# Optimization experiments

Measured on AMD Instinct MI355X. Metric: run time of the kernel, lower is better.

Reference implementation:

```python
import jax, jax.numpy as jnp
import numpy as np

# Dimensions (see shape_source)
S = 32          # frames
P = 196         # tokens per frame (14x14 patches)
H = 16          # heads
D = 64          # head dim
C = H * D       # 1024
N = S * P       # 6272
B = 1
K_NEAREST = 10
MK = K_NEAREST * P  # max gathered KV tokens per frame (padded)
LN_EPS = 1e-6


def _build_covis_gather(rng):
    """Build [S, MK] gather indices + padding bias from a ragged covisibility mask,
    mirroring SparseAttentionAggregator._build_gather_index."""
    gather_idx = np.zeros((S, MK), dtype=np.int32)
    attn_bias = np.zeros((S, MK), dtype=np.float32)
    arange_p = np.arange(P)
    for i in range(S):
        k_i = int(rng.integers(4, K_NEAREST + 1))  # variable-size covisible set
        others = rng.choice(np.delete(np.arange(S), i), size=k_i - 1, replace=False)
        covis = np.sort(np.concatenate([[i], others]))  # always includes self
        tok = (covis[:, None] * P + arange_p[None, :]).reshape(-1)  # [k_i*P]
        gather_idx[i, : tok.size] = tok
        if tok.size < MK:
            gather_idx[i, tok.size:] = tok[0]   # pad with a valid token
            attn_bias[i, tok.size:] = -1e9      # mask padded positions
    return gather_idx, attn_bias


def setup_inputs() -> dict:
    key = jax.random.key(0)
    kx, kqkv, kproj = jax.random.split(key, 3)
    rng = np.random.default_rng(0)
    gather_idx, attn_bias = _build_covis_gather(rng)
    w_scale = 0.02
    return {
        "x": jax.random.normal(kx, (B, N, C), dtype=jnp.float32),
        "W_qkv": w_scale * jax.random.normal(kqkv, (C, 3 * C), dtype=jnp.float32),
        "b_qkv": jnp.zeros((3 * C,), dtype=jnp.float32),
        "q_gamma": jnp.ones((D,), dtype=jnp.float32),
        "q_beta": jnp.zeros((D,), dtype=jnp.float32),
        "k_gamma": jnp.ones((D,), dtype=jnp.float32),
        "k_beta": jnp.zeros((D,), dtype=jnp.float32),
        "W_proj": w_scale * jax.random.normal(kproj, (C, C), dtype=jnp.float32),
        "b_proj": jnp.zeros((C,), dtype=jnp.float32),
        "gather_idx": jnp.asarray(gather_idx),
        "attn_bias": jnp.asarray(attn_bias),
    }


def _layernorm(t, gamma, beta):
    # LayerNorm over the last (head) dim, as q_norm / k_norm
    mu = jnp.mean(t, axis=-1, keepdims=True)
    var = jnp.mean(jnp.square(t - mu), axis=-1, keepdims=True)
    return (t - mu) * jax.lax.rsqrt(var + LN_EPS) * gamma + beta


def reference(x, W_qkv, b_qkv, q_gamma, q_beta, k_gamma, k_beta, W_proj, b_proj,
              gather_idx, attn_bias):
    Bx, Nx, Cx = x.shape
    mk = gather_idx.shape[1]
    # qkv projection -> q, k, v as [B, H, N, D]
    qkv = (x @ W_qkv + b_qkv).reshape(Bx, Nx, 3, H, D)
    q = jnp.transpose(qkv[:, :, 0], (0, 2, 1, 3))
    k = jnp.transpose(qkv[:, :, 1], (0, 2, 1, 3))
    v = jnp.transpose(qkv[:, :, 2], (0, 2, 1, 3))
    q = _layernorm(q, q_gamma, q_beta)
    k = _layernorm(k, k_gamma, k_beta)
    # single gather of all covisible K/V tokens: [B, H, S*MK, D] -> [B, S, H, MK, D]
    flat_idx = gather_idx.reshape(-1)
    kf = jnp.transpose(k[:, :, flat_idx, :].reshape(Bx, H, S, mk, D), (0, 2, 1, 3, 4))
    vf = jnp.transpose(v[:, :, flat_idx, :].reshape(Bx, H, S, mk, D), (0, 2, 1, 3, 4))
    # queries grouped per frame: [B, S, H, P, D]
    qb = jnp.transpose(q.reshape(Bx, H, S, P, D), (0, 2, 1, 3, 4))
    # batched SDPA over all frames at once
    scores = jnp.einsum('bshpd,bshmd->bshpm', qb, kf) * (D ** -0.5)
    scores = scores + attn_bias[None, :, None, None, :]
    attn = jax.nn.softmax(scores, axis=-1)
    out = jnp.einsum('bshpm,bshmd->bshpd', attn, vf)  # [B, S, H, P, D]
    # back to [B, N, C]
    out = jnp.transpose(out, (0, 2, 1, 3, 4)).reshape(Bx, H, Nx, D)
    out = jnp.transpose(out, (0, 2, 1, 3)).reshape(Bx, Nx, Cx)
    return out @ W_proj + b_proj
```

## Files before the change

### kernel.cpp

```cpp
#include <hip/hip_runtime.h>
#include <hip/hip_bf16.h>
#include <cstdint>
#include <cstddef>

#define S_FRAMES 32
#define P_TOK    196
#define H_HEADS  16
#define D_HEAD   64
#define C_DIM    1024
#define N_TOK    (S_FRAMES * P_TOK)
#define MK_TOK   1960
#define LN_EPS   1e-6f
#define SM_SCALE 0.125f

typedef __attribute__((ext_vector_type(8))) short short8;
typedef __attribute__((ext_vector_type(4))) short short4v;
typedef __attribute__((ext_vector_type(4))) float f32x4;

static __device__ __forceinline__ ushort f2bf(float x) {
  union { float f; unsigned u; } c; c.f = x;
  unsigned r = (c.u + 0x7FFFu + ((c.u >> 16) & 1u)) >> 16;
  return (ushort)r;
}
static __device__ __forceinline__ float bf2f(ushort h) {
  union { unsigned u; float f; } c; c.u = ((unsigned)h) << 16;
  return c.f;
}
static __device__ __forceinline__ unsigned pack_bf16x2(float a, float b) {
  union { float f; unsigned u; } x, y; x.f = a; y.f = b;
  unsigned lo = (x.u + 0x7FFFu + ((x.u >> 16) & 1u)) >> 16;
  unsigned hi = (y.u + 0x7FFFu + ((y.u >> 16) & 1u)) >> 16;
  return lo | (hi << 16);
}

#define GLOAD16(g, l) __builtin_amdgcn_global_load_lds( \
    (const __attribute__((address_space(1))) void*)(g), \
    (__attribute__((address_space(3))) void*)(l), 16, 0, 0)

__global__ __launch_bounds__(256) void wsplit_kernel(
    const float* __restrict__ W, ushort* __restrict__ Bth,
    ushort* __restrict__ Btl, int K, int Nn)
{
  __shared__ float T[64][72];
  const int n0 = blockIdx.x * 64;
  const int k0 = blockIdx.y * 64;
  const int tid = threadIdx.x;

  for (int idx = tid; idx < 64 * 16; idx += 256) {
    int r = idx >> 4, c4 = idx & 15;
    *(float4*)&T[r][c4 * 4] = *(const float4*)(W + (size_t)(k0 + r) * Nn + n0 + c4 * 4);
  }
  __syncthreads();
  for (int idx = tid; idx < 64 * 8; idx += 256) {
    int nr = idx >> 3, ch = idx & 7;
    short8 hi, lo;
    #pragma unroll
    for (int u = 0; u < 8; ++u) {
      float v = T[ch * 8 + u][nr];
      ushort h = f2bf(v);
      hi[u] = (short)h;
      lo[u] = (short)f2bf(v - bf2f(h));
    }
    *(short8*)(Bth + (size_t)(n0 + nr) * K + k0 + ch * 8) = hi;
    *(short8*)(Btl + (size_t)(n0 + nr) * K + k0 + ch * 8) = lo;
  }
}

__global__ __launch_bounds__(256) void xsplit_kernel(
    const float* __restrict__ x, ushort* __restrict__ Xh,
    ushort* __restrict__ Xl, int n4)
{
  for (int i = blockIdx.x * 256 + threadIdx.x; i < n4; i += gridDim.x * 256) {
    float4 v = ((const float4*)x)[i];
    float vv[4] = {v.x, v.y, v.z, v.w};
    short4v h, lo;
    #pragma unroll
    for (int u = 0; u < 4; ++u) {
      ushort hb = f2bf(vv[u]);
      h[u] = (short)hb;
      lo[u] = (short)f2bf(vv[u] - bf2f(hb));
    }
    ((short4v*)Xh)[i] = h;
    ((short4v*)Xl)[i] = lo;
  }
}

template <int EMODE>
__global__ __launch_bounds__(256, 2) void gemm_split3(
    const ushort* __restrict__ Ah_g, const ushort* __restrict__ Al_g,
    const ushort* __restrict__ Bth, const ushort* __restrict__ Btl,
    const float* __restrict__ bias, float* __restrict__ Cout,
    ushort* __restrict__ Qb, ushort* __restrict__ Kb, ushort* __restrict__ Vtg,
    const float* __restrict__ qg, const float* __restrict__ qbet,
    const float* __restrict__ kg, const float* __restrict__ kbet,
    int M, int Nn, int K)
{
  __shared__ ushort Ah[128 * 64];
  __shared__ ushort Al[128 * 64];
  __shared__ ushort Bh[128 * 64];
  __shared__ ushort Bl[128 * 64];

  const int tid  = threadIdx.x;
  const int wave = tid >> 6;
  const int lane = tid & 63;
  const int g    = lane >> 4;
  const int lq   = lane & 15;
  const int bm   = blockIdx.y * 128;
  const int bn   = blockIdx.x * 128;
  const int wm   = (wave >> 1) * 64;
  const int wn   = (wave & 1) * 64;

  size_t offA[4], offB[4];
  unsigned ldsoff[4];
  #pragma unroll
  for (int i = 0; i < 4; ++i) {
    const int tr = wave * 8 + i * 32 + (lane >> 3);
    const int gc = (lane & 7) ^ (tr & 7);
    offA[i] = (size_t)(bm + tr) * K + gc * 8;
    offB[i] = (size_t)(bn + tr) * K + gc * 8;
    ldsoff[i] = (unsigned)(wave * 512 + i * 2048);
  }

  f32x4 acc[4][4];
  #pragma unroll
  for (int i = 0; i < 4; ++i)
    #pragma unroll
    for (int j = 0; j < 4; ++j) {
      acc[i][j][0] = 0.f; acc[i][j][1] = 0.f;
      acc[i][j][2] = 0.f; acc[i][j][3] = 0.f;
    }

  for (int k0 = 0; k0 < K; k0 += 64) {
    __syncthreads();
    #pragma unroll
    for (int i = 0; i < 4; ++i) {
      GLOAD16(Ah_g + offA[i] + k0, &Ah[ldsoff[i]]);
      GLOAD16(Al_g + offA[i] + k0, &Al[ldsoff[i]]);
      GLOAD16(Bth  + offB[i] + k0, &Bh[ldsoff[i]]);
      GLOAD16(Btl  + offB[i] + k0, &Bl[ldsoff[i]]);
    }
    __syncthreads();

    #pragma unroll
    for (int kt = 0; kt < 2; ++kt) {
      short8 ah[4], al[4], bh[4], bl[4];
      #pragma unroll
      for (int mi = 0; mi < 4; ++mi) {
        const int row = wm + mi * 16 + lq;
        const int sl = (kt * 4 + g) ^ (row & 7);
        ah[mi] = *(const short8*)&Ah[row * 64 + sl * 8];
        al[mi] = *(const short8*)&Al[row * 64 + sl * 8];
      }
      #pragma unroll
      for (int ni = 0; ni < 4; ++ni) {
        const int row = wn + ni * 16 + lq;
        const int sl = (kt * 4 + g) ^ (row & 7);
        bh[ni] = *(const short8*)&Bh[row * 64 + sl * 8];
        bl[ni] = *(const short8*)&Bl[row * 64 + sl * 8];
      }
      #pragma unroll
      for (int mi = 0; mi < 4; ++mi)
        #pragma unroll
        for (int ni = 0; ni < 4; ++ni) {
          acc[mi][ni] = __builtin_amdgcn_mfma_f32_16x16x32_bf16(ah[mi], bl[ni], acc[mi][ni], 0, 0, 0);
          acc[mi][ni] = __builtin_amdgcn_mfma_f32_16x16x32_bf16(al[mi], bh[ni], acc[mi][ni], 0, 0, 0);
          acc[mi][ni] = __builtin_amdgcn_mfma_f32_16x16x32_bf16(ah[mi], bh[ni], acc[mi][ni], 0, 0, 0);
        }
    }
  }

  const int col0 = bn + wn;
  float bias4[4];
  #pragma unroll
  for (int ni = 0; ni < 4; ++ni) bias4[ni] = bias[col0 + ni * 16 + lq];

  if (EMODE == 0) {
    #pragma unroll
    for (int mi = 0; mi < 4; ++mi)
      #pragma unroll
      for (int r = 0; r < 4; ++r) {
        float* cp = Cout + (size_t)(bm + wm + mi * 16 + g * 4 + r) * Nn + col0;
        #pragma unroll
        for (int ni = 0; ni < 4; ++ni)
          cp[ni * 16 + lq] = acc[mi][ni][r] + bias4[ni];
      }
  } else {
    const int type = col0 >> 10;
    const int h    = (col0 & 1023) >> 6;
    if (type < 2) {
      const float* gam = type ? kg : qg;
      const float* bet = type ? kbet : qbet;
      float gm[4], bt[4];
      #pragma unroll
      for (int ni = 0; ni < 4; ++ni) {
        gm[ni] = gam[ni * 16 + lq];
        bt[ni] = bet[ni * 16 + lq];
      }
      ushort* outb = (type ? Kb : Qb);
      #pragma unroll
      for (int mi = 0; mi < 4; ++mi)
        #pragma unroll
        for (int r = 0; r < 4; ++r) {
          float xv[4];
          float s = 0.f;
          #pragma unroll
          for (int ni = 0; ni < 4; ++ni) {
            xv[ni] = acc[mi][ni][r] + bias4[ni];
            s += xv[ni];
          }
          s += __shfl_xor(s, 1, 64);
          s += __shfl_xor(s, 2, 64);
          s += __shfl_xor(s, 4, 64);
          s += __shfl_xor(s, 8, 64);
          const float mu = s * (1.0f / 64.0f);
          float ss = 0.f;
          #pragma unroll
          for (int ni = 0; ni < 4; ++ni) {
            float dd = xv[ni] - mu;
            ss += dd * dd;
          }
          ss += __shfl_xor(ss, 1, 64);
          ss += __shfl_xor(ss, 2, 64);
          ss += __shfl_xor(ss, 4, 64);
          ss += __shfl_xor(ss, 8, 64);
          const float rs = rsqrtf(ss * (1.0f / 64.0f) + LN_EPS);
          const int tok = bm + wm + mi * 16 + g * 4 + r;
          ushort* op = outb + ((size_t)h * N_TOK + tok) * 64;
          #pragma unroll
          for (int ni = 0; ni < 4; ++ni)
            op[ni * 16 + lq] = f2bf((xv[ni] - mu) * rs * gm[ni] + bt[ni]);
        }
    } else {
      #pragma unroll
      for (int mi = 0; mi < 4; ++mi) {
        const int tok = bm + wm + mi * 16 + g * 4;
        #pragma unroll
        for (int ni = 0; ni < 4; ++ni) {
          const int d = ni * 16 + lq;
          short4v w;
          #pragma unroll
          for (int r = 0; r < 4; ++r) w[r] = (short)f2bf(acc[mi][ni][r] + bias4[ni]);
          *(short4v*)&Vtg[((size_t)(h * 64 + d)) * N_TOK + tok] = w;
        }
      }
    }
  }
}

__global__ __launch_bounds__(512, 2) void attn_mfma_kernel(
    const ushort* __restrict__ Qb, const ushort* __restrict__ Kb,
    const ushort* __restrict__ Vtg,
    const int* __restrict__ gather_idx, const float* __restrict__ attn_bias,
    ushort* __restrict__ Chi, ushort* __restrict__ Clo)
{
  constexpr int KROWS = 224;
  constexpr int VROW  = 232;
  constexpr int PROW  = 40;
  __shared__ ushort Ks[KROWS * 64];
  __shared__ ushort Vs[64 * VROW];
  __shared__ ushort Pl[8][16 * PROW];

  const int s = blockIdx.x >> 4;
  const int h = blockIdx.x & 15;
  const int tid = threadIdx.x;
  const int wave = tid >> 6;
  const int lane = tid & 63;
  const int g  = lane >> 4;
  const int lq = lane & 15;
  const int nq = (wave < 5) ? 2 : 1;

  const float KEXP = 0.18033688011112042f;
  const float BEXP = 11.541560327111708f;

  for (int c = tid; c < (KROWS - P_TOK) * 8; c += 512) {
    const int row = P_TOK + (c >> 3), ch = c & 7;
    short8 z = {0,0,0,0,0,0,0,0};
    *(short8*)&Ks[row * 64 + (ch << 3)] = z;
  }
  for (int c = tid; c < 64 * 7; c += 512) {
    const int d = c / 7, ch = 49 + (c % 7);
    short4v z = {0,0,0,0};
    *(short4v*)&Vs[d * VROW + (ch << 2)] = z;
  }

  f32x4 oacc[2][4];
  #pragma unroll
  for (int t = 0; t < 2; ++t)
    #pragma unroll
    for (int dt = 0; dt < 4; ++dt) {
      oacc[t][dt][0] = 0.f; oacc[t][dt][1] = 0.f;
      oacc[t][dt][2] = 0.f; oacc[t][dt][3] = 0.f;
    }
  float lsum[2] = {0.f, 0.f};

  for (int f = 0; f < 10; ++f) {
    if (attn_bias[(size_t)s * MK_TOK + f * P_TOK] < -1.0e8f) break;
    const int tok0 = gather_idx[(size_t)s * MK_TOK + f * P_TOK];
    __syncthreads();

    for (int c = tid; c < P_TOK * 8; c += 512) {
      const int row = c >> 3, ch = c & 7;
      *(short8*)&Ks[row * 64 + ((ch ^ (row & 7)) << 3)] =
          *(const short8*)(Kb + ((size_t)h * N_TOK + tok0 + row) * 64 + (ch << 3));
    }
    for (int c = tid; c < 64 * 49; c += 512) {
      const int d = c / 49, ch = c - d * 49;
      *(short4v*)&Vs[d * VROW + (ch << 2)] =
          *(const short4v*)(Vtg + ((size_t)(h * 64 + d)) * N_TOK + tok0 + (ch << 2));
    }
    __syncthreads();

    #pragma unroll
    for (int t = 0; t < 2; ++t) {
      if (t >= nq) break;
      const int qt = wave + t * 8;
      int qrow = qt * 16 + lq; if (qrow > P_TOK - 1) qrow = P_TOK - 1;
      const ushort* qbase = Qb + ((size_t)h * N_TOK + s * P_TOK + qrow) * 64 + g * 8;
      const short8 qf0 = *(const short8*)(qbase);
      const short8 qf1 = *(const short8*)(qbase + 32);

      for (int kt2 = 0; kt2 < 7; ++kt2) {
        #pragma unroll
        for (int half = 0; half < 2; ++half) {
          const int kt = kt2 * 2 + half;
          f32x4 sacc = {0.f, 0.f, 0.f, 0.f};
          if (kt < 13) {
            const int row = kt * 16 + lq;
            const int sw = row & 7;
            short8 ka0 = *(const short8*)&Ks[row * 64 + ((g ^ sw) << 3)];
            short8 ka1 = *(const short8*)&Ks[row * 64 + (((4 + g) ^ sw) << 3)];
            sacc = __builtin_amdgcn_mfma_f32_16x16x32_bf16(ka0, qf0, sacc, 0, 0, 0);
            sacc = __builtin_amdgcn_mfma_f32_16x16x32_bf16(ka1, qf1, sacc, 0, 0, 0);
          }
          float p[4];
          #pragma unroll
          for (int r = 0; r < 4; ++r) {
            const int kv = kt * 16 + g * 4 + r;
            float e = __builtin_exp2f(fmaf(sacc[r], KEXP, -BEXP));
            p[r] = (kv < P_TOK) ? e : 0.f;
            lsum[t] += p[r];
          }
          ushort* pw = &Pl[wave][lq * PROW + half * 16 + g * 4];
          *(unsigned*)(pw)     = pack_bf16x2(p[0], p[1]);
          *(unsigned*)(pw + 2) = pack_bf16x2(p[2], p[3]);
        }
        const short8 pa = *(const short8*)&Pl[wave][lq * PROW + g * 8];
        #pragma unroll
        for (int dt = 0; dt < 4; ++dt) {
          const short8 vb = *(const short8*)&Vs[(dt * 16 + lq) * VROW + kt2 * 32 + g * 8];
          oacc[t][dt] = __builtin_amdgcn_mfma_f32_16x16x32_bf16(pa, vb, oacc[t][dt], 0, 0, 0);
        }
      }
    }
  }

  #pragma unroll
  for (int t = 0; t < 2; ++t) {
    if (t >= nq) break;
    const int qt = wave + t * 8;
    float lv = lsum[t];
    lv += __shfl_xor(lv, 16, 64);
    lv += __shfl_xor(lv, 32, 64);
    #pragma unroll
    for (int r = 0; r < 4; ++r) {
      const int qrow = qt * 16 + g * 4 + r;
      const float lr = __shfl(lv, (lane & 48) | (g * 4 + r), 64);
      const float inv = 1.0f / lr;
      if (qrow < P_TOK) {
        const size_t rowb = ((size_t)(s * P_TOK + qrow)) * C_DIM + h * 64;
        #pragma unroll
        for (int dt = 0; dt < 4; ++dt) {
          float val = oacc[t][dt][r] * inv;
          ushort hi = f2bf(val);
          Chi[rowb + dt * 16 + lq] = hi;
          Clo[rowb + dt * 16 + lq] = f2bf(val - bf2f(hi));
        }
      }
    }
  }
}

__global__ __launch_bounds__(256) void sgemm_bias_kernel(
    const float* __restrict__ A, const float* __restrict__ B,
    const float* __restrict__ bias, float* __restrict__ C,
    int M, int N, int K)
{
  constexpr int BM = 64, BN = 64, BK = 16;
  __shared__ alignas(16) float As[BK][BM + 4];
  __shared__ alignas(16) float Bs[BK][BN + 4];

  const int tid = threadIdx.x;
  const int bm = blockIdx.y * BM;
  const int bn = blockIdx.x * BN;
  const int tx = tid & 15;
  const int ty = tid >> 4;
  const int ar = tid >> 2;
  const int ak = (tid & 3) * 4;
  const int br = tid >> 4;
  const int bc = (tid & 15) * 4;

  float acc[4][4] = {};

  for (int k0 = 0; k0 < K; k0 += BK) {
    __syncthreads();
    float4 av = *(const float4*)(A + (size_t)(bm + ar) * K + k0 + ak);
    As[ak + 0][ar] = av.x;
    As[ak + 1][ar] = av.y;
    As[ak + 2][ar] = av.z;
    As[ak + 3][ar] = av.w;
    *(float4*)&Bs[br][bc] = *(const float4*)(B + (size_t)(k0 + br) * N + bn + bc);
    __syncthreads();

    #pragma unroll
    for (int kk = 0; kk < BK; ++kk) {
      float4 a4 = *(const float4*)&As[kk][ty * 4];
      float4 b4 = *(const float4*)&Bs[kk][tx * 4];
      float aa[4] = {a4.x, a4.y, a4.z, a4.w};
      float bb[4] = {b4.x, b4.y, b4.z, b4.w};
      #pragma unroll
      for (int i = 0; i < 4; ++i)
        #pragma unroll
        for (int j = 0; j < 4; ++j)
          acc[i][j] = fmaf(aa[i], bb[j], acc[i][j]);
    }
  }

  #pragma unroll
  for (int i = 0; i < 4; ++i) {
    float4 o;
    o.x = acc[i][0] + bias[bn + tx * 4 + 0];
    o.y = acc[i][1] + bias[bn + tx * 4 + 1];
    o.z = acc[i][2] + bias[bn + tx * 4 + 2];
    o.w = acc[i][3] + bias[bn + tx * 4 + 3];
    *(float4*)(C + (size_t)(bm + ty * 4 + i) * N + bn + tx * 4) = o;
  }
}

__global__ __launch_bounds__(128) void qk_ln_kernel(
    float* __restrict__ qkv,
    const float* __restrict__ qg, const float* __restrict__ qb,
    const float* __restrict__ kg, const float* __restrict__ kb)
{
  const int r = blockIdx.x;
  const int n = r / H_HEADS;
  const int h = r % H_HEADS;
  const int wave = threadIdx.x >> 6;
  const int lane = threadIdx.x & 63;

  float* p = qkv + (size_t)n * (3 * C_DIM) + wave * C_DIM + h * D_HEAD + lane;
  float v = *p;
  float sum = v;
  #pragma unroll
  for (int off = 32; off; off >>= 1) sum += __shfl_xor(sum, off, 64);
  float mu = sum * (1.0f / 64.0f);
  float d = v - mu;
  float vs = d * d;
  #pragma unroll
  for (int off = 32; off; off >>= 1) vs += __shfl_xor(vs, off, 64);
  float var = vs * (1.0f / 64.0f);
  float rstd = rsqrtf(var + LN_EPS);
  const float* gg = wave ? kg : qg;
  const float* bb = wave ? kb : qb;
  *p = d * rstd * gg[lane] + bb[lane];
}

__global__ __launch_bounds__(256) void sparse_attn_kernel(
    const float* __restrict__ qkv,
    const int*   __restrict__ gather_idx,
    const float* __restrict__ attn_bias,
    float* __restrict__ attn_out)
{
  constexpr int KC = 64;
  __shared__ alignas(16) float Ksf[KC][D_HEAD + 4];
  __shared__ alignas(16) float Vsf[KC][D_HEAD + 4];
  __shared__ float biasS[KC];

  const int s = blockIdx.x >> 4;
  const int h = blockIdx.x & 15;
  const int tid = threadIdx.x;
  const int p = tid;
  const bool active = (p < P_TOK);

  const int*   gi = gather_idx + (size_t)s * MK_TOK;
  const float* bi = attn_bias + (size_t)s * MK_TOK;

  const int qrow = s * P_TOK + (active ? p : 0);
  const float* qptr = qkv + (size_t)qrow * (3 * C_DIM) + h * D_HEAD;
  float q[D_HEAD];
  #pragma unroll
  for (int c = 0; c < 16; ++c) {
    float4 t4 = *(const float4*)(qptr + 4 * c);
    q[4 * c + 0] = t4.x; q[4 * c + 1] = t4.y;
    q[4 * c + 2] = t4.z; q[4 * c + 3] = t4.w;
  }

  float m = -3.0e38f;
  float l = 0.0f;
  float acc[D_HEAD] = {};
  const int jld = tid & 63;
  const int cpart = tid >> 6;

  for (int j0 = 0; j0 < MK_TOK; j0 += KC) {
    const int jn = min(KC, MK_TOK - j0);
    __syncthreads();
    if (jld < jn) {
      const int idx = gi[j0 + jld];
      const float* kbp = qkv + (size_t)idx * (3 * C_DIM) + C_DIM + h * D_HEAD + cpart * 16;
      const float* vbp = kbp + C_DIM;
      #pragma unroll
      for (int u = 0; u < 4; ++u) {
        *(float4*)&Ksf[jld][cpart * 16 + 4 * u] = *(const float4*)(kbp + 4 * u);
        *(float4*)&Vsf[jld][cpart * 16 + 4 * u] = *(const float4*)(vbp + 4 * u);
      }
    }
    if (tid < jn) biasS[tid] = bi[j0 + tid];
    __syncthreads();

    for (int j = 0; j < jn; ++j) {
      float s0 = 0.f, s1 = 0.f, s2 = 0.f, s3 = 0.f;
      #pragma unroll
      for (int c = 0; c < 16; ++c) {
        float4 kv = *(const float4*)&Ksf[j][4 * c];
        s0 = fmaf(q[4 * c + 0], kv.x, s0);
        s1 = fmaf(q[4 * c + 1], kv.y, s1);
        s2 = fmaf(q[4 * c + 2], kv.z, s2);
        s3 = fmaf(q[4 * c + 3], kv.w, s3);
      }
      float sc = (s0 + s1) + (s2 + s3);
      sc = sc * SM_SCALE + biasS[j];
      if (sc > m) {
        float al = __expf(m - sc);
        l *= al;
        #pragma unroll
        for (int d = 0; d < D_HEAD; ++d) acc[d] *= al;
        m = sc;
      }
      float pe = __expf(sc - m);
      l += pe;
      #pragma unroll
      for (int c = 0; c < 16; ++c) {
        float4 vv = *(const float4*)&Vsf[j][4 * c];
        acc[4 * c + 0] = fmaf(pe, vv.x, acc[4 * c + 0]);
        acc[4 * c + 1] = fmaf(pe, vv.y, acc[4 * c + 1]);
        acc[4 * c + 2] = fmaf(pe, vv.z, acc[4 * c + 2]);
        acc[4 * c + 3] = fmaf(pe, vv.w, acc[4 * c + 3]);
      }
    }
  }

  if (active) {
    const float inv = 1.0f / l;
    float* op = attn_out + (size_t)(s * P_TOK + p) * C_DIM + h * D_HEAD;
    #pragma unroll
    for (int c = 0; c < 16; ++c) {
      float4 o;
      o.x = acc[4 * c + 0] * inv;
      o.y = acc[4 * c + 1] * inv;
      o.z = acc[4 * c + 2] * inv;
      o.w = acc[4 * c + 3] * inv;
      *(float4*)(op + 4 * c) = o;
    }
  }
}

extern "C" void kernel_launch(void* const* d_in, const int* in_sizes, int n_in,
                              void* d_out, int out_size, void* d_ws, size_t ws_size,
                              hipStream_t stream)
{
  const float* x      = (const float*)d_in[0];
  const float* W_qkv  = (const float*)d_in[1];
  const float* b_qkv  = (const float*)d_in[2];
  const float* q_g    = (const float*)d_in[3];
  const float* q_b    = (const float*)d_in[4];
  const float* k_g    = (const float*)d_in[5];
  const float* k_b    = (const float*)d_in[6];
  const float* W_proj = (const float*)d_in[7];
  const float* b_proj = (const float*)d_in[8];
  const int*   g_idx  = (const int*)d_in[9];
  const float* a_bias = (const float*)d_in[10];
  float* out = (float*)d_out;

  const size_t VS = (size_t)H_HEADS * D_HEAD * N_TOK;
  const size_t WQ = (size_t)3 * C_DIM * C_DIM;
  const size_t WP = (size_t)C_DIM * C_DIM;
  const size_t need_new = (5 * VS + 2 * WQ + 2 * WP) * sizeof(ushort);

  if (ws_size >= need_new) {
    ushort* base = (ushort*)d_ws;
    ushort* Vtg  = base;
    ushort* Qb   = base + VS;
    ushort* Kb   = base + 2 * VS;
    ushort* Chi  = base + 3 * VS;
    ushort* Clo  = base + 4 * VS;
    ushort* WqT_h = base + 5 * VS;
    ushort* WqT_l = WqT_h + WQ;
    ushort* WpT_h = WqT_l + WQ;
    ushort* WpT_l = WpT_h + WP;
    ushort* Xh = Chi;
    ushort* Xl = Clo;

    wsplit_kernel<<<dim3(48, 16), 256, 0, stream>>>(W_qkv, WqT_h, WqT_l, C_DIM, 3 * C_DIM);
    wsplit_kernel<<<dim3(16, 16), 256, 0, stream>>>(W_proj, WpT_h, WpT_l, C_DIM, C_DIM);
    xsplit_kernel<<<2048, 256, 0, stream>>>(x, Xh, Xl, N_TOK * C_DIM / 4);

    gemm_split3<1><<<dim3(24, 49), 256, 0, stream>>>(
        Xh, Xl, WqT_h, WqT_l, b_qkv, nullptr,
        Qb, Kb, Vtg, q_g, q_b, k_g, k_b, N_TOK, 3 * C_DIM, C_DIM);

    attn_mfma_kernel<<<S_FRAMES * H_HEADS, 512, 0, stream>>>(
        Qb, Kb, Vtg, g_idx, a_bias, Chi, Clo);

    gemm_split3<0><<<dim3(8, 49), 256, 0, stream>>>(
        Chi, Clo, WpT_h, WpT_l, b_proj, out,
        nullptr, nullptr, nullptr, nullptr, nullptr, nullptr, nullptr,
        N_TOK, C_DIM, C_DIM);
  } else {
    float* qkv      = (float*)d_ws;
    float* attn_out = qkv + (size_t)N_TOK * 3 * C_DIM;
    sgemm_bias_kernel<<<dim3((3 * C_DIM) / 64, N_TOK / 64), 256, 0, stream>>>(
        x, W_qkv, b_qkv, qkv, N_TOK, 3 * C_DIM, C_DIM);
    qk_ln_kernel<<<N_TOK * H_HEADS, 128, 0, stream>>>(qkv, q_g, q_b, k_g, k_b);
    sparse_attn_kernel<<<S_FRAMES * H_HEADS, 256, 0, stream>>>(
        qkv, g_idx, a_bias, attn_out);
    sgemm_bias_kernel<<<dim3(C_DIM / 64, N_TOK / 64), 256, 0, stream>>>(
        attn_out, W_proj, b_proj, out, N_TOK, C_DIM, C_DIM);
  }
}
```

Before: 436.1 us.

## Schedule attention blocks longest-first and streamline softmax packing in attention kernel

After: 478.9 us. +9.8%, slower.

```diff
diff --git a/kernel.cpp b/kernel.cpp
--- a/kernel.cpp
+++ b/kernel.cpp
@@ -26,11 +26,10 @@
   union { unsigned u; float f; } c; c.u = ((unsigned)h) << 16;
   return c.f;
 }
-static __device__ __forceinline__ unsigned pack_bf16x2(float a, float b) {
-  union { float f; unsigned u; } x, y; x.f = a; y.f = b;
-  unsigned lo = (x.u + 0x7FFFu + ((x.u >> 16) & 1u)) >> 16;
-  unsigned hi = (y.u + 0x7FFFu + ((y.u >> 16) & 1u)) >> 16;
-  return lo | (hi << 16);
+static __device__ __forceinline__ unsigned pack_cvt(float a, float b) {
+  unsigned r;
+  asm("v_cvt_pk_bf16_f32 %0, %1, %2" : "=v"(r) : "v"(a), "v"(b));
+  return r;
 }
 
 #define GLOAD16(g, l) __builtin_amdgcn_global_load_lds( \
@@ -82,6 +81,32 @@
     }
     ((short4v*)Xh)[i] = h;
     ((short4v*)Xl)[i] = lo;
+  }
+}
+
+__global__ void sched_kernel(const float* __restrict__ ab, int* __restrict__ order)
+{
+  __shared__ int cnt[32];
+  __shared__ int idxs[32];
+  const int t = threadIdx.x;
+  if (t < 32) {
+    int c = 0;
+    for (int f = 0; f < 10; ++f) {
+      if (ab[(size_t)t * MK_TOK + f * P_TOK] < -1.0e8f) break;
+      ++c;
+    }
+    cnt[t] = c;
+    idxs[t] = t;
+  }
+  __syncthreads();
+  if (t == 0) {
+    for (int i = 0; i < 31; ++i) {
+      int best = i;
+      for (int j = i + 1; j < 32; ++j)
+        if (cnt[idxs[j]] > cnt[idxs[best]]) best = j;
+      int tmp = idxs[i]; idxs[i] = idxs[best]; idxs[best] = tmp;
+    }
+    for (int i = 0; i < 32; ++i) order[i] = idxs[i];
   }
 }
 
@@ -251,16 +276,17 @@
     const ushort* __restrict__ Qb, const ushort* __restrict__ Kb,
     const ushort* __restrict__ Vtg,
     const int* __restrict__ gather_idx, const float* __restrict__ attn_bias,
+    const int* __restrict__ order,
     ushort* __restrict__ Chi, ushort* __restrict__ Clo)
 {
-  constexpr int KROWS = 224;
+  constexpr int KROWS = 208;
   constexpr int VROW  = 232;
   constexpr int PROW  = 40;
   __shared__ ushort Ks[KROWS * 64];
   __shared__ ushort Vs[64 * VROW];
-  __shared__ ushort Pl[8][16 * PROW];
-
-  const int s = blockIdx.x >> 4;
+  __shared__ ushort Pl[8][2][16 * PROW];
+
+  const int s = order[blockIdx.x >> 4];
   const int h = blockIdx.x & 15;
   const int tid = threadIdx.x;
   const int wave = tid >> 6;
@@ -283,6 +309,17 @@
     *(short4v*)&Vs[d * VROW + (ch << 2)] = z;
   }
 
+  short8 qf0[2], qf1[2];
+  #pragma unroll 2
+  for (int t = 0; t < 2; ++t) {
+    if (t >= nq) break;
+    const int qt = wave + t * 8;
+    int qrow = qt * 16 + lq; if (qrow > P_TOK - 1) qrow = P_TOK - 1;
+    const ushort* qbase = Qb + ((size_t)h * N_TOK + s * P_TOK + qrow) * 64 + g * 8;
+    qf0[t] = *(const short8*)(qbase);
+    qf1[t] = *(const short8*)(qbase + 32);
+  }
+
   f32x4 oacc[2][4];
   #pragma unroll
   for (int t = 0; t < 2; ++t)
@@ -310,16 +347,12 @@
     }
     __syncthreads();
 
-    #pragma unroll
+    #pragma unroll 2
     for (int t = 0; t < 2; ++t) {
       if (t >= nq) break;
-      const int qt = wave + t * 8;
-      int qrow = qt * 16 + lq; if (qrow > P_TOK - 1) qrow = P_TOK - 1;
-      const ushort* qbase = Qb + ((size_t)h * N_TOK + s * P_TOK + qrow) * 64 + g * 8;
-      const short8 qf0 = *(const short8*)(qbase);
-      const short8 qf1 = *(const short8*)(qbase + 32);
 
       for (int kt2 = 0; kt2 < 7; ++kt2) {
+        const int pbuf = kt2 & 1;
         #pragma unroll
         for (int half = 0; half < 2; ++half) {
           const int kt = kt2 * 2 + half;
@@ -329,22 +362,24 @@
             const int sw = row & 7;
             short8 ka0 = *(const short8*)&Ks[row * 64 + ((g ^ sw) << 3)];
             short8 ka1 = *(const short8*)&Ks[row * 64 + (((4 + g) ^ sw) << 3)];
-            sacc = __builtin_amdgcn_mfma_f32_16x16x32_bf16(ka0, qf0, sacc, 0, 0, 0);
-            sacc = __builtin_amdgcn_mfma_f32_16x16x32_bf16(ka1, qf1, sacc, 0, 0, 0);
+            sacc = __builtin_amdgcn_mfma_f32_16x16x32_bf16(ka0, qf0[t], sacc, 0, 0, 0);
+            sacc = __builtin_amdgcn_mfma_f32_16x16x32_bf16(ka1, qf1[t], sacc, 0, 0, 0);
           }
           float p[4];
           #pragma unroll
-          for (int r = 0; r < 4; ++r) {
-            const int kv = kt * 16 + g * 4 + r;
-            float e = __builtin_exp2f(fmaf(sacc[r], KEXP, -BEXP));
-            p[r] = (kv < P_TOK) ? e : 0.f;
-            lsum[t] += p[r];
+          for (int r = 0; r < 4; ++r)
+            p[r] = __builtin_exp2f(fmaf(sacc[r], KEXP, -BEXP));
+          if (kt2 == 6) {
+            #pragma unroll
+            for (int r = 0; r < 4; ++r)
+              if (kt * 16 + g * 4 + r >= P_TOK) p[r] = 0.f;
           }
-          ushort* pw = &Pl[wave][lq * PROW + half * 16 + g * 4];
-          *(unsigned*)(pw)     = pack_bf16x2(p[0], p[1]);
-          *(unsigned*)(pw + 2) = pack_bf16x2(p[2], p[3]);
+          lsum[t] += (p[0] + p[1]) + (p[2] + p[3]);
+          ushort* pw = &Pl[wave][pbuf][lq * PROW + half * 16 + g * 4];
+          *(unsigned*)(pw)     = pack_cvt(p[0], p[1]);
+          *(unsigned*)(pw + 2) = pack_cvt(p[2], p[3]);
         }
-        const short8 pa = *(const short8*)&Pl[wave][lq * PROW + g * 8];
+        const short8 pa = *(const short8*)&Pl[wave][pbuf][lq * PROW + g * 8];
         #pragma unroll
         for (int dt = 0; dt < 4; ++dt) {
           const short8 vb = *(const short8*)&Vs[(dt * 16 + lq) * VROW + kt2 * 32 + g * 8];
@@ -354,7 +389,7 @@
     }
   }
 
-  #pragma unroll
+  #pragma unroll 2
   for (int t = 0; t < 2; ++t) {
     if (t >= nq) break;
     const int qt = wave + t * 8;
@@ -583,7 +618,7 @@
   const size_t VS = (size_t)H_HEADS * D_HEAD * N_TOK;
   const size_t WQ = (size_t)3 * C_DIM * C_DIM;
   const size_t WP = (size_t)C_DIM * C_DIM;
-  const size_t need_new = (5 * VS + 2 * WQ + 2 * WP) * sizeof(ushort);
+  const size_t need_new = (5 * VS + 2 * WQ + 2 * WP) * sizeof(ushort) + 256;
 
   if (ws_size >= need_new) {
     ushort* base = (ushort*)d_ws;
@@ -596,19 +631,21 @@
     ushort* WqT_l = WqT_h + WQ;
     ushort* WpT_h = WqT_l + WQ;
     ushort* WpT_l = WpT_h + WP;
+    int*    order = (int*)(WpT_l + WP);
     ushort* Xh = Chi;
     ushort* Xl = Clo;
 
     wsplit_kernel<<<dim3(48, 16), 256, 0, stream>>>(W_qkv, WqT_h, WqT_l, C_DIM, 3 * C_DIM);
     wsplit_kernel<<<dim3(16, 16), 256, 0, stream>>>(W_proj, WpT_h, WpT_l, C_DIM, C_DIM);
     xsplit_kernel<<<2048, 256, 0, stream>>>(x, Xh, Xl, N_TOK * C_DIM / 4);
+    sched_kernel<<<1, 64, 0, stream>>>(a_bias, order);
 
     gemm_split3<1><<<dim3(24, 49), 256, 0, stream>>>(
         Xh, Xl, WqT_h, WqT_l, b_qkv, nullptr,
         Qb, Kb, Vtg, q_g, q_b, k_g, k_b, N_TOK, 3 * C_DIM, C_DIM);
 
     attn_mfma_kernel<<<S_FRAMES * H_HEADS, 512, 0, stream>>>(
-        Qb, Kb, Vtg, g_idx, a_bias, Chi, Clo);
+        Qb, Kb, Vtg, g_idx, a_bias, order, Chi, Clo);
 
     gemm_split3<0><<<dim3(8, 49), 256, 0, stream>>>(
         Chi, Clo, WpT_h, WpT_l, b_proj, out,
```
